# Kernel tuning notes

Measured on AMD Instinct MI355X. Metric: run time of the kernel, lower is better.

## Reference

```python
import jax, jax.numpy as jnp
import numpy as np
import math

NEG = -1e9


def maximum_path(logp, mask):
    # logp, mask: [B, Tx, Ty]; Viterbi-style monotonic alignment search (VITS MAS)
    B, Tx, Ty = logp.shape
    lp = jnp.where(mask > 0, logp, NEG)
    # forward DP: value[x, y] = lp[x, y] + max(value[x, y-1], value[x-1, y-1])
    v0 = jnp.where(jnp.arange(Tx)[None, :] == 0, lp[:, :, 0], NEG)  # [B, Tx]

    def fwd(v, lp_y):
        v_diag = jnp.pad(v[:, :-1], ((0, 0), (1, 0)), constant_values=NEG)
        take_diag = v_diag > v  # strict >, matches cython 'value[x,y-1] < value[x-1,y-1]'
        return lp_y + jnp.maximum(v, v_diag), take_diag

    lp_rest = jnp.moveaxis(lp[:, :, 1:], 2, 0)  # [Ty-1, B, Tx]
    _, dirs = jax.lax.scan(fwd, v0, lp_rest)
    dirs = jnp.concatenate([jnp.zeros((1, B, Tx), bool), dirs], axis=0)  # [Ty, B, Tx]

    t_x = mask[:, :, 0].sum(axis=1).astype(jnp.int32)  # valid text length per batch
    t_y = mask[:, 0, :].sum(axis=1).astype(jnp.int32)  # valid spec length per batch

    def back(idx, inp):
        dir_y, y = inp  # dir_y [B, Tx], y scalar
        active = (y < t_y)  # [B]
        row = jax.nn.one_hot(idx, Tx, dtype=logp.dtype) * active[:, None].astype(logp.dtype)
        d = jnp.take_along_axis(dir_y, idx[:, None], axis=1)[:, 0]
        idx = jnp.where(active, idx - d.astype(jnp.int32), idx)
        return idx, row

    ys = jnp.arange(Ty - 1, -1, -1)
    _, rows = jax.lax.scan(back, t_x - 1, (dirs[::-1], ys))
    path = jnp.moveaxis(rows[::-1], 0, 2)  # [B, Tx, Ty]
    return path


def _make_masks(x_lengths, y_lengths, Tx, Ty):
    x_len = jnp.clip(x_lengths, 2, Tx)
    y_len = jnp.clip(y_lengths, 2, Ty)
    y_len = jnp.maximum(y_len, x_len)  # MAS needs T_y >= T_x per sample
    x_mask = (jnp.arange(Tx)[None, :] < x_len[:, None]).astype(jnp.float32)  # [B, Tx]
    y_mask = (jnp.arange(Ty)[None, :] < y_len[:, None]).astype(jnp.float32)  # [B, Ty]
    return x_mask, y_mask


def setup_inputs() -> dict:
    key = jax.random.key(0)
    B, C, Tx, Ty = 32, 192, 512, 2048
    k1, k2, k3, k4, k5 = jax.random.split(key, 5)
    z_p = jax.random.normal(k1, (B, C, Ty), dtype=jnp.float32)
    m_p = jax.random.normal(k2, (B, C, Tx), dtype=jnp.float32)
    logs_p = jax.random.normal(k3, (B, C, Tx), dtype=jnp.float32) * 0.3
    x_lengths = jax.random.randint(k4, (B,), Tx // 2, Tx + 1, dtype=jnp.int32)
    y_lengths = jax.random.randint(k5, (B,), Ty // 2, Ty + 1, dtype=jnp.int32)
    return {"z_p": z_p, "m_p": m_p, "logs_p": logs_p, "x_lengths": x_lengths, "y_lengths": y_lengths}


def reference(z_p, m_p, logs_p, x_lengths, y_lengths):
    B, C, Ty = z_p.shape
    Tx = m_p.shape[2]
    x_mask, y_mask = _make_masks(x_lengths, y_lengths, Tx, Ty)
    attn_mask = x_mask[:, :, None] * y_mask[:, None, :]  # [B, Tx, Ty]

    # log N(z_p ; m_p, exp(logs_p)) scored for every (text, spec) pair
    o_scale = jnp.exp(-2.0 * logs_p)  # [B, C, Tx]
    logp1 = jnp.sum(-0.5 * math.log(2.0 * math.pi) - logs_p, axis=1)[:, :, None]  # [B, Tx, 1]
    logp2 = jnp.einsum('bct,bcs->bts', o_scale, -0.5 * z_p ** 2)  # [B, Tx, Ty]
    logp3 = jnp.einsum('bct,bcs->bts', m_p * o_scale, z_p)
    logp4 = jnp.sum(-0.5 * m_p ** 2 * o_scale, axis=1)[:, :, None]
    logp = logp2 + logp3 + logp1 + logp4

    attn = maximum_path(logp, attn_mask)  # [B, Tx, Ty], hard 0/1 alignment
    attn_durations = attn.sum(axis=2)[:, None, :]  # [B, 1, Tx]

    # expand text stats to spec frames: torch.einsum('klmn,kjm->kjn', attn[:,None], m_p)
    m_p_dur = jnp.einsum('bts,bct->bcs', attn, m_p)      # [B, C, Ty]
    logs_p_dur = jnp.einsum('bts,bct->bcs', attn, logs_p)
    return attn_durations, attn[:, None], m_p_dur, logs_p_dur
```

## Files before the change

### kernel.cpp

```cpp
#include <hip/hip_runtime.h>

#define NEGV -1e9f
#define BB 32
#define CC 192
#define TXD 512
#define TYD 2048

#define E_DUR   0
#define E_ATTN  16384
#define E_MP    33570816
#define E_LS    46153728
#define E_TOTAL 58736640

#define OFF_DIRS  6291456

#define WS_PATH 0ull
#define WS_YST  131072ull
#define WS_TXTY 196864ull
#define WS_NEED 262144ull

typedef _Float16 f16x8 __attribute__((ext_vector_type(8)));
typedef float f32x4 __attribute__((ext_vector_type(4)));

__device__ __forceinline__ void glds16(const void* g, void* l) {
    __builtin_amdgcn_global_load_lds((const __attribute__((address_space(1))) unsigned*)g,
                                     (__attribute__((address_space(3))) unsigned*)l, 16, 0, 0);
}
__device__ __forceinline__ unsigned packh(_Float16 a, _Float16 b) {
    union { _Float16 h[2]; unsigned u; } x; x.h[0] = a; x.h[1] = b; return x.u;
}

__global__ __launch_bounds__(256) void k_prepB(const float* __restrict__ logs_p,
                                               const float* __restrict__ m_p,
                                               const int* __restrict__ xl,
                                               const int* __restrict__ yl,
                                               _Float16* __restrict__ Bpl,
                                               float* __restrict__ l14,
                                               unsigned* __restrict__ txty) {
    __shared__ float lst[CC][33];
    __shared__ float mst[CC][33];
    __shared__ float p14[8][32];
    int b = blockIdx.y, t0 = blockIdx.x * 32, tid = threadIdx.x;
    const float* lsb = logs_p + (size_t)b * CC * TXD + t0;
    const float* mb  = m_p    + (size_t)b * CC * TXD + t0;
#pragma unroll
    for (int i = 0; i < 24; ++i) {
        int u = i * 256 + tid, c = u >> 5, t = u & 31;
        lst[c][t] = lsb[(size_t)c * TXD + t];
        mst[c][t] = mb [(size_t)c * TXD + t];
    }
    __syncthreads();
    { int q = tid >> 5, t = tid & 31; float s = 0.f;
      for (int c = q * 24; c < q * 24 + 24; ++c) {
          float ls = lst[c][t], m = mst[c][t];
          float o = expf(-2.f * ls);
          s += -0.918938533204672741780329736406f - ls - 0.5f * m * m * o;
      }
      p14[q][t] = s; }
    __syncthreads();
    if (tid < 32) {
        float s = 0.f;
#pragma unroll
        for (int q = 0; q < 8; ++q) s += p14[q][tid];
        l14[b * TXD + t0 + tid] = s;
    }
    _Float16* Bb = Bpl + (size_t)b * (4 * TXD * CC);
    unsigned* B0 = (unsigned*)(Bb);
    unsigned* B1 = (unsigned*)(Bb + (size_t)1 * TXD * CC);
    unsigned* B2 = (unsigned*)(Bb + (size_t)2 * TXD * CC);
    unsigned* B3 = (unsigned*)(Bb + (size_t)3 * TXD * CC);
#pragma unroll
    for (int i = 0; i < 12; ++i) {
        int u = i * 256 + tid, t = u / 96, cp = u - t * 96, c = cp * 2;
        float ls0 = lst[c][t], ls1 = lst[c + 1][t];
        float m0 = mst[c][t], m1 = mst[c + 1][t];
        float o0 = expf(-2.f * ls0), o1 = expf(-2.f * ls1);
        float w0 = m0 * o0, w1 = m1 * o1;
        _Float16 oh0 = (_Float16)o0, oh1 = (_Float16)o1;
        _Float16 ol0 = (_Float16)(o0 - (float)oh0), ol1 = (_Float16)(o1 - (float)oh1);
        _Float16 wh0 = (_Float16)w0, wh1 = (_Float16)w1;
        _Float16 wl0 = (_Float16)(w0 - (float)wh0), wl1 = (_Float16)(w1 - (float)wh1);
        int ui = ((t0 + t) * CC + c) >> 1;
        B0[ui] = packh(oh0, oh1);
        B1[ui] = packh(ol0, ol1);
        B2[ui] = packh(wh0, wh1);
        B3[ui] = packh(wl0, wl1);
    }
    if (blockIdx.x == 0 && blockIdx.y == 0 && tid < BB) {
        int txv = min(max(xl[tid], 2), TXD);
        int tyv = min(max(yl[tid], 2), TYD);
        tyv = max(tyv, txv);
        txty[tid] = (unsigned)txv;
        txty[BB + tid] = (unsigned)tyv;
    }
}

__global__ __launch_bounds__(256) void k_prepZ(const float* __restrict__ z_p,
                                               _Float16* __restrict__ Zpl, int sBase) {
    __shared__ float zt[CC][65];
    int b = blockIdx.y, s0 = blockIdx.x * 64, tid = threadIdx.x;
    const float* zb = z_p + (size_t)b * CC * TYD + sBase + s0;
#pragma unroll
    for (int i = 0; i < 48; ++i) {
        int u = i * 256 + tid, c = u >> 6, s = u & 63;
        zt[c][s] = zb[(size_t)c * TYD + s];
    }
    __syncthreads();
    _Float16* Zb = Zpl + (size_t)b * (4 * 1024 * CC);
    unsigned* Z0 = (unsigned*)(Zb);
    unsigned* Z1 = (unsigned*)(Zb + (size_t)1 * 1024 * CC);
    unsigned* Z2 = (unsigned*)(Zb + (size_t)2 * 1024 * CC);
    unsigned* Z3 = (unsigned*)(Zb + (size_t)3 * 1024 * CC);
#pragma unroll
    for (int i = 0; i < 24; ++i) {
        int u = i * 256 + tid, s = u / 96, cp = u - s * 96, c = cp * 2;
        float z0 = zt[c][s], z1 = zt[c + 1][s];
        float P0 = -0.5f * z0 * z0, P1 = -0.5f * z1 * z1;
        _Float16 ph0 = (_Float16)P0, ph1 = (_Float16)P1;
        _Float16 pl0 = (_Float16)(P0 - (float)ph0), pl1 = (_Float16)(P1 - (float)ph1);
        _Float16 zh0 = (_Float16)z0, zh1 = (_Float16)z1;
        _Float16 zl0 = (_Float16)(z0 - (float)zh0), zl1 = (_Float16)(z1 - (float)zh1);
        int ui = ((s0 + s) * CC + c) >> 1;
        Z0[ui] = packh(ph0, ph1);
        Z1[ui] = packh(pl0, pl1);
        Z2[ui] = packh(zh0, zh1);
        Z3[ui] = packh(zl0, zl1);
    }
}

__global__ __launch_bounds__(256, 2) void k_mm(const _Float16* __restrict__ Zpl,
                                               const _Float16* __restrict__ Bpl,
                                               const float* __restrict__ l14,
                                               const unsigned* __restrict__ txty,
                                               float* __restrict__ L, int sBase) {
    __shared__ __align__(16) char As[32768];
    __shared__ __align__(16) char Bs[16384];
    int bid = blockIdx.x;
    int xcd = bid & 7, idx = bid >> 3;
    int b = xcd + 8 * (idx >> 4);
    int tile = idx & 15;
    int s0 = (tile >> 2) * 256, t0 = (tile & 3) * 128;
    int txb = (int)txty[b], tyb = (int)txty[BB + b];
    int sg0 = sBase + s0;
    if (sg0 >= tyb) return;
    int tid = threadIdx.x, l = tid & 63, w = tid >> 6;
    float* Lt = L + ((size_t)b * TYD + sg0) * TXD + t0;
    if (t0 >= txb) {
#pragma unroll
        for (int i = 0; i < 32; ++i) {
            int u = i * 256 + tid, r = u >> 5, c4 = (u & 31) * 4;
            *(float4*)(Lt + (size_t)r * TXD + c4) = make_float4(NEGV, NEGV, NEGV, NEGV);
        }
        return;
    }
    f32x4 acc[4][8];
#pragma unroll
    for (int i = 0; i < 4; ++i)
#pragma unroll
        for (int j = 0; j < 8; ++j) acc[i][j] = (f32x4){0.f, 0.f, 0.f, 0.f};

    const char* Zb = (const char*)(Zpl + (size_t)b * (4 * 1024 * CC));
    const char* Bb = (const char*)(Bpl + (size_t)b * (4 * TXD * CC));
    int lrow = l >> 3;
    int gOff = lrow * 384 + (((l & 7) ^ lrow) * 16);
    int arow_off = (w * 64 + (l & 15)) * 128;
    int brow_off = (l & 15) * 128;
    int slot0 = (((l >> 4) + 0) ^ (l & 7)) * 16;
    int slot1 = (((l >> 4) + 4) ^ (l & 7)) * 16;

    for (int pass = 0; pass < 6; ++pass) {
        int ap = ((pass >= 3) ? 2 : 0) + ((pass == 2 || pass == 5) ? 1 : 0);
        int bp = ((pass >= 3) ? 2 : 0) + ((pass == 1 || pass == 4) ? 1 : 0);
        const char* Zp = Zb + ((size_t)ap * 1024 + s0) * 384;
        const char* Bp = Bb + ((size_t)bp * TXD + t0) * 384;
        for (int k0 = 0; k0 < 384; k0 += 128) {
            __syncthreads();
#pragma unroll
            for (int j = 0; j < 8; ++j) {
                int c = w * 8 + j;
                glds16(Zp + (size_t)c * (8 * 384) + gOff + k0, As + c * 1024);
            }
#pragma unroll
            for (int j = 0; j < 4; ++j) {
                int c = w * 4 + j;
                glds16(Bp + (size_t)c * (8 * 384) + gOff + k0, Bs + c * 1024);
            }
            __syncthreads();
#pragma unroll
            for (int ks = 0; ks < 2; ++ks) {
                int so = ks ? slot1 : slot0;
                f16x8 av[4], bv[8];
#pragma unroll
                for (int fm = 0; fm < 4; ++fm)
                    av[fm] = *(const f16x8*)(As + arow_off + fm * (16 * 128) + so);
#pragma unroll
                for (int fn = 0; fn < 8; ++fn)
                    bv[fn] = *(const f16x8*)(Bs + brow_off + fn * (16 * 128) + so);
#pragma unroll
                for (int fm = 0; fm < 4; ++fm)
#pragma unroll
                    for (int fn = 0; fn < 8; ++fn)
                        acc[fm][fn] = __builtin_amdgcn_mfma_f32_16x16x32_f16(
                            av[fm], bv[fn], acc[fm][fn], 0, 0, 0);
            }
        }
    }
    float l14v[8];
#pragma unroll
    for (int fn = 0; fn < 8; ++fn) l14v[fn] = l14[b * TXD + t0 + fn * 16 + (l & 15)];
    int sb = sg0 + w * 64 + (l >> 4) * 4;
    int tcol = t0 + (l & 15);
#pragma unroll
    for (int fm = 0; fm < 4; ++fm)
#pragma unroll
        for (int r = 0; r < 4; ++r) {
            int sg = sb + fm * 16 + r;
            bool sv = sg < tyb;
            float* Lrow = L + ((size_t)b * TYD + sg) * TXD;
#pragma unroll
            for (int fn = 0; fn < 8; ++fn) {
                int t = tcol + fn * 16;
                Lrow[t] = (sv && t < txb) ? (acc[fm][fn][r] + l14v[fn]) : NEGV;
            }
        }
}

__global__ __launch_bounds__(128) void k_dp(const float* __restrict__ L,
                                            const unsigned* __restrict__ txty,
                                            unsigned* __restrict__ dirsG,
                                            unsigned short* __restrict__ pathG,
                                            unsigned* __restrict__ ystartG,
                                            float* __restrict__ outDur) {
    __shared__ __align__(16) float ring[32 * 512];
    __shared__ unsigned char dmaps[32 * 512];
    __shared__ unsigned short path[TYD];
    __shared__ unsigned cnt[513];
    __shared__ unsigned ebuf[32];
    int b = blockIdx.x, tid = threadIdx.x;
    int lane = tid & 63, wid = tid >> 6;
    int tx = (int)txty[b], ty = (int)txty[BB + b];
    const char* Lb = (const char*)(L + (size_t)b * (TYD * TXD));
    unsigned* dGw = dirsG + (size_t)b * (512 * 64);
    int G = (ty + 3) >> 2;

    if (wid == 1) {
        int c0s = lane ^ ((lane >> 3) & 7);
        int srcOff0 = c0s * 16;
        int srcOff1 = srcOff0 + 1024;
#pragma unroll
        for (int g = 0; g < 6; ++g) {
#pragma unroll
            for (int q = 0; q < 4; ++q) {
                int r = 4 * g + q;
                int rc = min(r, ty - 1);
                const char* src = Lb + (size_t)rc * 2048;
                char* dst = (char*)&ring[(r & 31) * 512];
                glds16(src + srcOff0, dst);
                glds16(src + srcOff1, dst + 1024);
            }
        }
        for (int g = 0; g < G; ++g) {
            asm volatile("s_waitcnt vmcnt(40)" ::: "memory");
            __builtin_amdgcn_s_barrier();
            __builtin_amdgcn_sched_barrier(0);
            int gs = g + 6;
#pragma unroll
            for (int q = 0; q < 4; ++q) {
                int r = 4 * gs + q;
                int rc = min(r, ty - 1);
                const char* src = Lb + (size_t)rc * 2048;
                char* dst = (char*)&ring[(r & 31) * 512];
                glds16(src + srcOff0, dst);
                glds16(src + srcOff1, dst + 1024);
            }
        }
    } else {
        int sl0 = (2 * lane) ^ ((lane >> 2) & 7);
        int sl1 = sl0 ^ 1;
        float v[8];
        unsigned p[8];
        for (int g = 0; g < G; ++g) {
            __builtin_amdgcn_s_barrier();
            __builtin_amdgcn_sched_barrier(0);
            float4 lo[4], hi[4];
#pragma unroll
            for (int q = 0; q < 4; ++q) {
                const char* rr = (const char*)&ring[((4 * g + q) & 31) * 512];
                lo[q] = *(const float4*)(rr + sl0 * 16);
                hi[q] = *(const float4*)(rr + sl1 * 16);
            }
            unsigned dbits = 0;
#pragma unroll
            for (int q = 0; q < 4; ++q) {
                int y = 4 * g + q;
                if (y == 0) {
                    float lp[8] = {lo[0].x, lo[0].y, lo[0].z, lo[0].w,
                                   hi[0].x, hi[0].y, hi[0].z, hi[0].w};
#pragma unroll
                    for (int i = 0; i < 8; ++i) {
                        int x = lane * 8 + i;
                        v[i] = (x == 0) ? lp[i] : NEGV;
                        p[i] = (unsigned)x;
                    }
                } else if (y < ty) {
                    float cur[8] = {lo[q].x, lo[q].y, lo[q].z, lo[q].w,
                                    hi[q].x, hi[q].y, hi[q].z, hi[q].w};
                    float vp0 = __shfl_up(v[7], 1);
                    unsigned pp0 = (unsigned)__shfl_up((int)p[7], 1);
                    if (lane == 0) vp0 = NEGV;
                    unsigned bits = 0;
#pragma unroll
                    for (int i = 7; i >= 0; --i) {
                        float vp = (i == 0) ? vp0 : v[i - 1];
                        unsigned pp = (i == 0) ? pp0 : p[i - 1];
                        bool d = vp > v[i];
                        v[i] = cur[i] + (d ? vp : v[i]);
                        p[i] = d ? pp : p[i];
                        bits |= (d ? 1u : 0u) << i;
                    }
                    dbits |= bits << (8 * q);
                    if ((y & 63) == 0) {
#pragma unroll
                        for (int i = 0; i < 8; ++i) p[i] = (unsigned)(lane * 8 + i);
                    }
                    if ((y & 63) == 63) {
                        int c = y >> 6;
#pragma unroll
                        for (int i = 0; i < 8; ++i)
                            dmaps[c * 512 + lane * 8 + i] =
                                (unsigned char)((unsigned)(lane * 8 + i) - p[i]);
                    }
                }
            }
            dGw[g * 64 + lane] = dbits;
        }
    }
    asm volatile("s_waitcnt vmcnt(0)" ::: "memory");
    __syncthreads();

    int c0 = (ty - 1) >> 6;
    if (tid == 0) {
        int pos = tx - 1;
        for (int y = ty - 1; y >= (c0 << 6); --y) {
            path[y] = (unsigned short)pos;
            unsigned wv = dGw[(y >> 2) * 64 + (pos >> 3)];
            pos -= (int)((wv >> (((y & 3) << 3) | (pos & 7))) & 1u);
        }
        for (int c = c0 - 1; c >= 0; --c) {
            ebuf[c] = (unsigned)pos;
            int P = pos - (int)dmaps[c * 512 + pos];
            unsigned wv = dGw[(c << 4) * 64 + (P >> 3)];
            pos = P - (int)((wv >> (P & 7)) & 1u);
        }
    }
    __syncthreads();
    if (tid < c0) {
        int c = tid;
        int pos = (int)ebuf[c];
        for (int y = (c << 6) + 63; y >= (c << 6); --y) {
            path[y] = (unsigned short)pos;
            unsigned wv = dGw[(y >> 2) * 64 + (pos >> 3)];
            pos -= (int)((wv >> (((y & 3) << 3) | (pos & 7))) & 1u);
        }
    }
    __syncthreads();

    for (int i = tid; i < 513; i += 128) cnt[i] = 0;
    __syncthreads();
    for (int y = tid; y < ty; y += 128) atomicAdd(&cnt[path[y]], 1u);
    __syncthreads();

    if (wid == 0) {
        unsigned c8[8], lsum = 0;
#pragma unroll
        for (int i = 0; i < 8; ++i) {
            c8[i] = cnt[lane * 8 + i];
            lsum += c8[i];
        }
        unsigned incl = lsum;
        for (int d = 1; d < 64; d <<= 1) {
            unsigned t = (unsigned)__shfl_up((int)incl, d);
            if (lane >= d) incl += t;
        }
        unsigned run = incl - lsum;
#pragma unroll
        for (int i = 0; i < 8; ++i) {
            int x = lane * 8 + i;
            ystartG[b * 513 + x] = run;
            outDur[(size_t)b * TXD + x] = (float)c8[i];
            run += c8[i];
        }
        if (lane == 0) ystartG[b * 513 + 512] = (unsigned)ty;
    }
    for (int y = tid; y < ty; y += 128) pathG[b * TYD + y] = path[y];
}

__global__ __launch_bounds__(64) void k_attn(const unsigned* __restrict__ ystartG,
                                             float* __restrict__ out) {
    int x = blockIdx.x, b = blockIdx.y, lane = threadIdx.x;
    unsigned s0 = ystartG[b * 513 + x];
    unsigned s1 = ystartG[b * 513 + x + 1];
    float* row = out + E_ATTN + ((size_t)(b * TXD + x)) * TYD + lane * 32;
#pragma unroll
    for (int k = 0; k < 8; ++k) {
        unsigned y0 = (unsigned)(lane * 32 + k * 4);
        float4 o;
        o.x = (y0 + 0 >= s0 && y0 + 0 < s1) ? 1.0f : 0.0f;
        o.y = (y0 + 1 >= s0 && y0 + 1 < s1) ? 1.0f : 0.0f;
        o.z = (y0 + 2 >= s0 && y0 + 2 < s1) ? 1.0f : 0.0f;
        o.w = (y0 + 3 >= s0 && y0 + 3 < s1) ? 1.0f : 0.0f;
        *(float4*)(row + k * 4) = o;
    }
}

__global__ __launch_bounds__(256) void k_gather(const float* __restrict__ m_p,
                                                const float* __restrict__ logs_p,
                                                const unsigned short* __restrict__ pathG,
                                                const unsigned* __restrict__ txty,
                                                float* __restrict__ out) {
    __shared__ unsigned short px[64];
    int yc = blockIdx.x, b = blockIdx.y;
    int y0 = yc * 64, tid = threadIdx.x;
    int lane = tid & 63, w = tid >> 6;
    int ty = (int)txty[BB + b];
    if (tid < 64) px[tid] = (y0 + tid < ty) ? pathG[b * TYD + y0 + tid] : 0;
    __syncthreads();
    bool act = (y0 + lane) < ty;
    int xx = (int)px[lane];
    for (int c = w; c < CC; c += 4) {
        float mv = act ? m_p[((size_t)b * CC + c) * TXD + xx] : 0.0f;
        float lv = act ? logs_p[((size_t)b * CC + c) * TXD + xx] : 0.0f;
        size_t oidx = ((size_t)(b * CC + c)) * TYD + y0 + lane;
        out[E_MP + oidx] = mv;
        out[E_LS + oidx] = lv;
    }
}

extern "C" void kernel_launch(void* const* d_in, const int* in_sizes, int n_in,
                              void* d_out, int out_size, void* d_ws, size_t ws_size,
                              hipStream_t stream) {
    if (out_size < E_TOTAL) return;
    if (ws_size < WS_NEED) return;
    const float* z_p    = (const float*)d_in[0];
    const float* m_p    = (const float*)d_in[1];
    const float* logs_p = (const float*)d_in[2];
    const int* xl       = (const int*)d_in[3];
    const int* yl       = (const int*)d_in[4];
    float* out = (float*)d_out;
    char* ws = (char*)d_ws;

    float* l14            = out + E_DUR;
    float* L              = out + E_ATTN;
    _Float16* Zpl         = (_Float16*)(out + E_MP);
    _Float16* Bpl         = (_Float16*)(out + E_LS);
    unsigned* dirsG       = (unsigned*)(out + E_LS + OFF_DIRS);
    unsigned short* pathG = (unsigned short*)(ws + WS_PATH);
    unsigned* ystartG     = (unsigned*)(ws + WS_YST);
    unsigned* txty        = (unsigned*)(ws + WS_TXTY);

    hipLaunchKernelGGL(k_prepB, dim3(16, BB), dim3(256), 0, stream,
                       logs_p, m_p, xl, yl, Bpl, l14, txty);
    hipLaunchKernelGGL(k_prepZ, dim3(16, BB), dim3(256), 0, stream, z_p, Zpl, 0);
    hipLaunchKernelGGL(k_mm, dim3(512), dim3(256), 0, stream, Zpl, Bpl, l14, txty, L, 0);
    hipLaunchKernelGGL(k_prepZ, dim3(16, BB), dim3(256), 0, stream, z_p, Zpl, 1024);
    hipLaunchKernelGGL(k_mm, dim3(512), dim3(256), 0, stream, Zpl, Bpl, l14, txty, L, 1024);
    hipLaunchKernelGGL(k_dp, dim3(BB), dim3(128), 0, stream, L, txty, dirsG, pathG, ystartG, out + E_DUR);
    hipLaunchKernelGGL(k_attn, dim3(TXD, BB), dim3(64), 0, stream, ystartG, out);
    hipLaunchKernelGGL(k_gather, dim3(TYD / 64, BB), dim3(256), 0, stream, m_p, logs_p, pathG, txty, out);
}
```

Baseline: 606.7 us.

## Double-buffer DP ring reads in registers with 8-row groups and fewer barriers

The DP stage now processes 8 spectrogram rows per producer/consumer step instead of 4, which halves the number of workgroup barriers. The consumer wave prefetches the next group's LDS values into a second register buffer while computing the current group, so LDS read latency overlaps the serial DP chain. The producer keeps three groups in flight with an adjusted vmcnt wait. In exchange, register use rises (four arrays of eight float4), and the deeper ring scheduling must stay consistent with the barrier pairing.

Measured after the change: 559.6 us. -7.8%, faster.

```diff
diff --git a/kernel.cpp b/kernel.cpp
--- a/kernel.cpp
+++ b/kernel.cpp
@@ -241,99 +241,113 @@
     int tx = (int)txty[b], ty = (int)txty[BB + b];
     const char* Lb = (const char*)(L + (size_t)b * (TYD * TXD));
     unsigned* dGw = dirsG + (size_t)b * (512 * 64);
-    int G = (ty + 3) >> 2;
+    int G8 = (ty + 7) >> 3;
 
     if (wid == 1) {
         int c0s = lane ^ ((lane >> 3) & 7);
         int srcOff0 = c0s * 16;
         int srcOff1 = srcOff0 + 1024;
-#pragma unroll
-        for (int g = 0; g < 6; ++g) {
-#pragma unroll
-            for (int q = 0; q < 4; ++q) {
-                int r = 4 * g + q;
-                int rc = min(r, ty - 1);
-                const char* src = Lb + (size_t)rc * 2048;
-                char* dst = (char*)&ring[(r & 31) * 512];
-                glds16(src + srcOff0, dst);
-                glds16(src + srcOff1, dst + 1024);
-            }
-        }
-        for (int g = 0; g < G; ++g) {
-            asm volatile("s_waitcnt vmcnt(40)" ::: "memory");
+        char* ringc = (char*)ring;
+#define STAGE_GRP(GR) do {                                                  \
+        _Pragma("unroll")                                                   \
+        for (int q_ = 0; q_ < 8; ++q_) {                                    \
+            int r_ = 8 * (GR) + q_;                                         \
+            int rc_ = min(r_, ty - 1);                                      \
+            const char* src_ = Lb + (size_t)rc_ * 2048;                     \
+            char* dst_ = ringc + (size_t)(r_ & 31) * 2048;                  \
+            glds16(src_ + srcOff0, dst_);                                   \
+            glds16(src_ + srcOff1, dst_ + 1024);                            \
+        } } while (0)
+        STAGE_GRP(0); STAGE_GRP(1); STAGE_GRP(2);
+        asm volatile("s_waitcnt vmcnt(16)" ::: "memory");
+        __builtin_amdgcn_s_barrier();
+        for (int g = 0; g < G8; ++g) {
+            __builtin_amdgcn_sched_barrier(0);
+            STAGE_GRP(g + 3);
+            asm volatile("s_waitcnt vmcnt(16)" ::: "memory");
             __builtin_amdgcn_s_barrier();
-            __builtin_amdgcn_sched_barrier(0);
-            int gs = g + 6;
-#pragma unroll
-            for (int q = 0; q < 4; ++q) {
-                int r = 4 * gs + q;
-                int rc = min(r, ty - 1);
-                const char* src = Lb + (size_t)rc * 2048;
-                char* dst = (char*)&ring[(r & 31) * 512];
-                glds16(src + srcOff0, dst);
-                glds16(src + srcOff1, dst + 1024);
-            }
-        }
+        }
+#undef STAGE_GRP
     } else {
         int sl0 = (2 * lane) ^ ((lane >> 2) & 7);
         int sl1 = sl0 ^ 1;
+        const char* ringc = (const char*)ring;
         float v[8];
         unsigned p[8];
-        for (int g = 0; g < G; ++g) {
+        float4 loA[8], hiA[8], loB[8], hiB[8];
+#define READ_GRP(LO, HI, GN) do {                                           \
+        const char* rb_ = ringc + (((GN) & 3) << 14);                       \
+        _Pragma("unroll")                                                   \
+        for (int q_ = 0; q_ < 8; ++q_) {                                    \
+            LO[q_] = *(const float4*)(rb_ + q_ * 2048 + sl0 * 16);          \
+            HI[q_] = *(const float4*)(rb_ + q_ * 2048 + sl1 * 16);          \
+        } } while (0)
+#define DP_GRP(LO, HI, G_) do {                                             \
+        unsigned w0_ = 0, w1_ = 0;                                          \
+        _Pragma("unroll")                                                   \
+        for (int q_ = 0; q_ < 8; ++q_) {                                    \
+            int y_ = 8 * (G_) + q_;                                         \
+            if ((G_) == 0 && q_ == 0) {                                     \
+                float lp_[8] = {LO[0].x, LO[0].y, LO[0].z, LO[0].w,         \
+                                HI[0].x, HI[0].y, HI[0].z, HI[0].w};        \
+                _Pragma("unroll")                                           \
+                for (int i = 0; i < 8; ++i) {                               \
+                    int x_ = lane * 8 + i;                                  \
+                    v[i] = (x_ == 0) ? lp_[i] : NEGV;                       \
+                    p[i] = (unsigned)x_;                                    \
+                }                                                           \
+            } else if (y_ < ty) {                                           \
+                float cur_[8] = {LO[q_].x, LO[q_].y, LO[q_].z, LO[q_].w,    \
+                                 HI[q_].x, HI[q_].y, HI[q_].z, HI[q_].w};   \
+                float vp0_ = __shfl_up(v[7], 1);                            \
+                unsigned pp0_ = (unsigned)__shfl_up((int)p[7], 1);          \
+                if (lane == 0) vp0_ = NEGV;                                 \
+                unsigned bits_ = 0;                                         \
+                _Pragma("unroll")                                           \
+                for (int i = 7; i >= 0; --i) {                              \
+                    float vp_ = (i == 0) ? vp0_ : v[i - 1];                 \
+                    unsigned pp_ = (i == 0) ? pp0_ : p[i - 1];              \
+                    bool d_ = vp_ > v[i];                                   \
+                    v[i] = cur_[i] + (d_ ? vp_ : v[i]);                     \
+                    p[i] = d_ ? pp_ : p[i];                                 \
+                    bits_ |= (d_ ? 1u : 0u) << i;                           \
+                }                                                           \
+                if (q_ < 4) w0_ |= bits_ << (8 * q_);                       \
+                else        w1_ |= bits_ << (8 * (q_ - 4));                 \
+                if (q_ == 0 && ((G_) & 7) == 0 && (G_) != 0) {              \
+                    _Pragma("unroll")                                       \
+                    for (int i = 0; i < 8; ++i) p[i] = (unsigned)(lane * 8 + i); \
+                }                                                           \
+                if (q_ == 7 && ((G_) & 7) == 7) {                           \
+                    int c_ = y_ >> 6;                                       \
+                    _Pragma("unroll")                                       \
+                    for (int i = 0; i < 8; ++i)                             \
+                        dmaps[c_ * 512 + lane * 8 + i] =                    \
+                            (unsigned char)((unsigned)(lane * 8 + i) - p[i]); \
+                }                                                           \
+            }                                                               \
+        }                                                                   \
+        dGw[(2 * (G_)) * 64 + lane] = w0_;                                  \
+        dGw[(2 * (G_) + 1) * 64 + lane] = w1_;                              \
+        } while (0)
+        __builtin_amdgcn_s_barrier();
+        __builtin_amdgcn_sched_barrier(0);
+        READ_GRP(loA, hiA, 0);
+        for (int g = 0; g < G8;) {
+            READ_GRP(loB, hiB, g + 1);
+            DP_GRP(loA, hiA, g);
+            ++g;
             __builtin_amdgcn_s_barrier();
             __builtin_amdgcn_sched_barrier(0);
-            float4 lo[4], hi[4];
-#pragma unroll
-            for (int q = 0; q < 4; ++q) {
-                const char* rr = (const char*)&ring[((4 * g + q) & 31) * 512];
-                lo[q] = *(const float4*)(rr + sl0 * 16);
-                hi[q] = *(const float4*)(rr + sl1 * 16);
-            }
-            unsigned dbits = 0;
-#pragma unroll
-            for (int q = 0; q < 4; ++q) {
-                int y = 4 * g + q;
-                if (y == 0) {
-                    float lp[8] = {lo[0].x, lo[0].y, lo[0].z, lo[0].w,
-                                   hi[0].x, hi[0].y, hi[0].z, hi[0].w};
-#pragma unroll
-                    for (int i = 0; i < 8; ++i) {
-                        int x = lane * 8 + i;
-                        v[i] = (x == 0) ? lp[i] : NEGV;
-                        p[i] = (unsigned)x;
-                    }
-                } else if (y < ty) {
-                    float cur[8] = {lo[q].x, lo[q].y, lo[q].z, lo[q].w,
-                                    hi[q].x, hi[q].y, hi[q].z, hi[q].w};
-                    float vp0 = __shfl_up(v[7], 1);
-                    unsigned pp0 = (unsigned)__shfl_up((int)p[7], 1);
-                    if (lane == 0) vp0 = NEGV;
-                    unsigned bits = 0;
-#pragma unroll
-                    for (int i = 7; i >= 0; --i) {
-                        float vp = (i == 0) ? vp0 : v[i - 1];
-                        unsigned pp = (i == 0) ? pp0 : p[i - 1];
-                        bool d = vp > v[i];
-                        v[i] = cur[i] + (d ? vp : v[i]);
-                        p[i] = d ? pp : p[i];
-                        bits |= (d ? 1u : 0u) << i;
-                    }
-                    dbits |= bits << (8 * q);
-                    if ((y & 63) == 0) {
-#pragma unroll
-                        for (int i = 0; i < 8; ++i) p[i] = (unsigned)(lane * 8 + i);
-                    }
-                    if ((y & 63) == 63) {
-                        int c = y >> 6;
-#pragma unroll
-                        for (int i = 0; i < 8; ++i)
-                            dmaps[c * 512 + lane * 8 + i] =
-                                (unsigned char)((unsigned)(lane * 8 + i) - p[i]);
-                    }
-                }
-            }
-            dGw[g * 64 + lane] = dbits;
-        }
+            if (g >= G8) break;
+            READ_GRP(loA, hiA, g + 1);
+            DP_GRP(loB, hiB, g);
+            ++g;
+            __builtin_amdgcn_s_barrier();
+            __builtin_amdgcn_sched_barrier(0);
+        }
+#undef READ_GRP
+#undef DP_GRP
     }
     asm volatile("s_waitcnt vmcnt(0)" ::: "memory");
     __syncthreads();
```
